# Kernel tuning notes

Measured on AMD Instinct MI355X. Metric: run time of the kernel, lower is better.

## Reference

```python
import jax, jax.numpy as jnp
import numpy as np
from jax import lax

WINDOW_SIZE = 11
SIGMA = 1.5
DATA_RANGE = 1.0
LEVELS = 4
EPS = 1e-8
DN = ('NCHW', 'OIHW', 'NCHW')


def _gauss1d(k, sigma):
    coords = jnp.arange(k, dtype=jnp.float32) - k // 2
    g = jnp.exp(-coords ** 2 / (2.0 * sigma ** 2))
    return g / g.sum()


def _blur(x, g):
    # separable depthwise Gaussian blur, VALID padding (use_padding=False)
    C = x.shape[1]
    k = g.shape[0]
    kw = jnp.broadcast_to(g.reshape(1, 1, 1, k), (C, 1, 1, k)).astype(x.dtype)
    kh = jnp.broadcast_to(g.reshape(1, 1, k, 1), (C, 1, k, 1)).astype(x.dtype)
    x = lax.conv_general_dilated(x, kw, (1, 1), 'VALID', dimension_numbers=DN, feature_group_count=C)
    x = lax.conv_general_dilated(x, kh, (1, 1), 'VALID', dimension_numbers=DN, feature_group_count=C)
    return x


def _avg_pool2(x):
    B, C, H, W = x.shape  # H, W even here (512 -> 64)
    return x.reshape(B, C, H // 2, 2, W // 2, 2).mean(axis=(3, 5))


def _ssim_level(X, Y, g):
    C1 = (0.01 * DATA_RANGE) ** 2
    C2 = (0.03 * DATA_RANGE) ** 2
    mu1 = _blur(X, g)
    mu2 = _blur(Y, g)
    sigma1_sq = _blur(X * X, g) - mu1 * mu1
    sigma2_sq = _blur(Y * Y, g) - mu2 * mu2
    sigma12 = _blur(X * Y, g) - mu1 * mu2
    cs_map = jax.nn.relu((2.0 * sigma12 + C2) / (sigma1_sq + sigma2_sq + C2))
    ssim_map = (2.0 * mu1 * mu2 + C1) / (mu1 * mu1 + mu2 * mu2 + C1) * cs_map
    return ssim_map.mean(axis=(1, 2, 3)), cs_map.mean(axis=(1, 2, 3))


def setup_inputs() -> dict:
    key = jax.random.key(0)
    kx, ky = jax.random.split(key)
    X = jax.random.uniform(kx, (16, 3, 512, 512), dtype=jnp.float32)
    Y = jax.random.uniform(ky, (16, 3, 512, 512), dtype=jnp.float32)
    return {'X': X, 'Y': Y}


def reference(X, Y):
    g = _gauss1d(WINDOW_SIZE, SIGMA)
    w = jnp.array([0.0448, 0.2856, 0.3001, 0.2363], dtype=jnp.float32)
    w = w / w.sum()
    vals = []
    for i in range(LEVELS):
        ss, cs = _ssim_level(X, Y, g)
        if i < LEVELS - 1:
            vals.append(cs)
            X = _avg_pool2(X)
            Y = _avg_pool2(Y)
        else:
            vals.append(ss)
    vals = jnp.maximum(jnp.stack(vals, axis=0), EPS)  # [levels, B]
    ms = jnp.prod(vals ** w[:, None], axis=0)
    return 1.0 - ms
```

## Files before the change

### kernel.cpp

```cpp
#include <hip/hip_runtime.h>
#include <math.h>

#define HALO 10
#define TS 32
#define IN 42
#define NP 21
#define XSTR 46
#define HSTR 46
#define NBIN 256

typedef float f2 __attribute__((ext_vector_type(2)));

struct GaussW { float g[11]; };


__global__ __launch_bounds__(256, 6) void ssim_level_kernel(
    const float* __restrict__ X, const float* __restrict__ Y,
    int H, GaussW gw, float* __restrict__ Plevel, int last_level,
    float* __restrict__ Xpool, float* __restrict__ Ypool)
{
    const int W = H;
    const int Hout = H - HALO;

    __shared__ float U[4 * TS * HSTR];
    __shared__ float red[4];
    float* Xs = U;
    float* Ys = U + IN * XSTR;

    const int tid = threadIdx.x;
    const int bc  = blockIdx.z;
    const int b   = bc / 3;
    const int r0  = blockIdx.y * TS;
    const int c0  = blockIdx.x * TS;
    const size_t base = (size_t)bc * H * W;

    for (int idx = tid; idx < IN * NP; idx += 256) {
        int rr = idx / NP, pp = idx - rr * NP;
        int gr = r0 + rr, gc = c0 + 2 * pp;
        float2 xv = make_float2(0.f, 0.f), yv = make_float2(0.f, 0.f);
        if (gr < H && gc < W) {
            const float* xp = X + base + (size_t)gr * W + gc;
            const float* yp = Y + base + (size_t)gr * W + gc;
            xv = *(const float2*)xp;
            yv = *(const float2*)yp;
        }
        *(float2*)&Xs[rr * XSTR + 2 * pp] = xv;
        *(float2*)&Ys[rr * XSTR + 2 * pp] = yv;
    }
    __syncthreads();

    float x[18], y[18];
    int rr = 0, ccb = 0;
    if (tid < 168) {
        rr  = tid >> 2;
        ccb = (tid & 3) * 8;
        #pragma unroll
        for (int u = 0; u < 9; ++u) {
            *(f2*)&x[2 * u] = *(const f2*)&Xs[rr * XSTR + ccb + 2 * u];
            *(f2*)&y[2 * u] = *(const f2*)&Ys[rr * XSTR + ccb + 2 * u];
        }
    } else if (tid >= 192 && !last_level) {
        const int t = tid - 192;
        const int Wp = W >> 1;
        #pragma unroll
        for (int q = 0; q < 4; ++q) {
            int cell = q * 64 + t;
            int pr = cell >> 4, pc = cell & 15;
            float2 xa = *(const float2*)&Xs[(2 * pr)     * XSTR + 2 * pc];
            float2 xb = *(const float2*)&Xs[(2 * pr + 1) * XSTR + 2 * pc];
            float2 ya = *(const float2*)&Ys[(2 * pr)     * XSTR + 2 * pc];
            float2 yb = *(const float2*)&Ys[(2 * pr + 1) * XSTR + 2 * pc];
            size_t o = (size_t)bc * (H >> 1) * Wp + (size_t)(r0 / 2 + pr) * Wp + (c0 / 2 + pc);
            Xpool[o] = 0.25f * (xa.x + xa.y + xb.x + xb.y);
            Ypool[o] = 0.25f * (ya.x + ya.y + yb.x + yb.y);
        }
    }
    __syncthreads();

    if (tid < 168) {
        #pragma unroll
        for (int p = 0; p < 4; ++p) {
            f2 ax = {0.f, 0.f}, ay = {0.f, 0.f};
            #pragma unroll
            for (int k = 0; k < 11; ++k) {
                f2 vx = { x[2 * p + k], x[2 * p + k + 1] };
                f2 vy = { y[2 * p + k], y[2 * p + k + 1] };
                ax += vx * gw.g[k];
                ay += vy * gw.g[k];
            }
            U[(0 * TS + ccb + 2 * p    ) * HSTR + rr] = ax.x;
            U[(0 * TS + ccb + 2 * p + 1) * HSTR + rr] = ax.y;
            U[(1 * TS + ccb + 2 * p    ) * HSTR + rr] = ay.x;
            U[(1 * TS + ccb + 2 * p + 1) * HSTR + rr] = ay.y;
        }
        #pragma unroll
        for (int i = 0; i < 9; ++i) {
            f2 xv = *(f2*)&x[2 * i];
            f2 yv = *(f2*)&y[2 * i];
            f2 a = xv + yv;
            f2 d = xv - yv;
            *(f2*)&x[2 * i] = a * a;
            *(f2*)&y[2 * i] = d * d;
        }
        #pragma unroll
        for (int p = 0; p < 4; ++p) {
            f2 as = {0.f, 0.f}, ad = {0.f, 0.f};
            #pragma unroll
            for (int k = 0; k < 11; ++k) {
                f2 vs = { x[2 * p + k], x[2 * p + k + 1] };
                f2 vd = { y[2 * p + k], y[2 * p + k + 1] };
                as += vs * gw.g[k];
                ad += vd * gw.g[k];
            }
            U[(2 * TS + ccb + 2 * p    ) * HSTR + rr] = as.x;
            U[(2 * TS + ccb + 2 * p + 1) * HSTR + rr] = as.y;
            U[(3 * TS + ccb + 2 * p    ) * HSTR + rr] = ad.x;
            U[(3 * TS + ccb + 2 * p + 1) * HSTR + rr] = ad.y;
        }
    }
    __syncthreads();

    const int tx = tid & 31;
    const int ty = tid >> 5;
    const int rb = ty * 4;

    f2 m1[2], m2[2], S[2], D[2];
    #define VPASS(Q, OUT)                                                        \
    {                                                                            \
        float win[14];                                                           \
        _Pragma("unroll")                                                        \
        for (int i = 0; i < 7; ++i)                                              \
            *(f2*)&win[2 * i] = *(const f2*)&U[(Q * TS + tx) * HSTR + rb + 2 * i]; \
        _Pragma("unroll")                                                        \
        for (int h = 0; h < 2; ++h) {                                            \
            f2 acc = {0.f, 0.f};                                                 \
            _Pragma("unroll")                                                    \
            for (int k = 0; k < 11; ++k) {                                       \
                f2 v = { win[2 * h + k], win[2 * h + k + 1] };                   \
                acc += v * gw.g[k];                                              \
            }                                                                    \
            OUT[h] = acc;                                                        \
        }                                                                        \
    }
    VPASS(0, m1) VPASS(1, m2) VPASS(2, S) VPASS(3, D)
    #undef VPASS

    const float C1 = 1e-4f, C2 = 9e-4f;
    float acc_s = 0.f;
    #pragma unroll
    for (int o = 0; o < 4; ++o) {
        float u1 = m1[o >> 1][o & 1], u2 = m2[o >> 1][o & 1];
        float Sv = S[o >> 1][o & 1],  Dv = D[o >> 1][o & 1];
        float u1s = u1 * u1, u2s = u2 * u2, u12 = u1 * u2;
        float ssum = 0.5f  * (Sv + Dv);
        float sxy  = 0.25f * (Sv - Dv);
        float vsum = ssum - u1s - u2s;
        float v12  = sxy - u12;
        float A2   = fmaxf(2.f * v12 + C2, 0.f);
        float B1   = u1s + u2s + C1;
        float B2   = vsum + C2;
        float inv  = __builtin_amdgcn_rcpf(B1 * B2);
        float val;
        if (!last_level) {
            val = A2 * B1 * inv;
        } else {
            float A1 = 2.f * u12 + C1;
            val = A1 * A2 * inv;
        }
        bool valid = (r0 + rb + o < Hout) && (c0 + tx < Hout);
        acc_s += valid ? val : 0.f;
    }

    #pragma unroll
    for (int off = 32; off; off >>= 1) acc_s += __shfl_down(acc_s, off);
    if ((tid & 63) == 0) red[tid >> 6] = acc_s;
    __syncthreads();
    if (tid == 0) {
        int lin = blockIdx.x + gridDim.x * (blockIdx.y + gridDim.y * blockIdx.z);
        int bin = lin & (NBIN - 1);
        atomicAdd(&Plevel[bin * 16 + b], red[0] + red[1] + red[2] + red[3]);
    }
}

__global__ void finalize_kernel(const float* __restrict__ P, float* __restrict__ out) {
    __shared__ float red[64][4];
    const int tid  = threadIdx.x;
    const int pair = tid >> 2;
    const int chnk = tid & 3;
    const int l = pair >> 4, b = pair & 15;
    float s = 0.f;
    #pragma unroll 4
    for (int j = 0; j < 64; ++j)
        s += P[((l * NBIN) + (chnk * 64) + j) * 16 + b];
    red[pair][chnk] = s;
    __syncthreads();
    if (tid < 16) {
        const int bb = tid;
        const float wraw[4] = {0.0448f, 0.2856f, 0.3001f, 0.2363f};
        float wsum = wraw[0] + wraw[1] + wraw[2] + wraw[3];
        float ms = 1.f;
        for (int ll = 0; ll < 4; ++ll) {
            int Hh = 512 >> ll;
            int Ho = Hh - HALO;
            float cnt = 3.f * (float)Ho * (float)Ho;
            float val = (red[ll * 16 + bb][0] + red[ll * 16 + bb][1] +
                         red[ll * 16 + bb][2] + red[ll * 16 + bb][3]) / cnt;
            val = fmaxf(val, 1e-8f);
            ms *= powf(val, wraw[ll] / wsum);
        }
        out[bb] = 1.f - ms;
    }
}

extern "C" void kernel_launch(void* const* d_in, const int* in_sizes, int n_in,
                              void* d_out, int out_size, void* d_ws, size_t ws_size,
                              hipStream_t stream)
{
    const float* X0 = (const float*)d_in[0];
    const float* Y0 = (const float*)d_in[1];
    float* out = (float*)d_out;
    float* ws  = (float*)d_ws;

    const size_t PSZ = (size_t)4 * NBIN * 16;
    float* P  = ws;
    float* X1 = ws + PSZ;
    float* Y1 = X1 + (size_t)16 * 3 * 256 * 256;
    float* X2 = Y1 + (size_t)16 * 3 * 256 * 256;
    float* Y2 = X2 + (size_t)16 * 3 * 128 * 128;
    float* X3 = Y2 + (size_t)16 * 3 * 128 * 128;
    float* Y3 = X3 + (size_t)16 * 3 * 64 * 64;

    GaussW gw;
    {
        float s = 0.f;
        for (int i = 0; i < 11; ++i) {
            float d = (float)(i - 5);
            gw.g[i] = expf(-d * d / (2.f * 1.5f * 1.5f));
            s += gw.g[i];
        }
        for (int i = 0; i < 11; ++i) gw.g[i] /= s;
    }

    hipMemsetAsync(P, 0, PSZ * sizeof(float), stream);

    hipLaunchKernelGGL(ssim_level_kernel, dim3(16, 16, 48), dim3(256), 0, stream,
                       X0, Y0, 512, gw, P + 0 * NBIN * 16, 0, X1, Y1);
    hipLaunchKernelGGL(ssim_level_kernel, dim3(8, 8, 48),   dim3(256), 0, stream,
                       X1, Y1, 256, gw, P + 1 * NBIN * 16, 0, X2, Y2);
    hipLaunchKernelGGL(ssim_level_kernel, dim3(4, 4, 48),   dim3(256), 0, stream,
                       X2, Y2, 128, gw, P + 2 * NBIN * 16, 0, X3, Y3);
    hipLaunchKernelGGL(ssim_level_kernel, dim3(2, 2, 48),   dim3(256), 0, stream,
                       X3, Y3, 64,  gw, P + 3 * NBIN * 16, 1, (float*)nullptr, (float*)nullptr);

    hipLaunchKernelGGL(finalize_kernel, dim3(1), dim3(256), 0, stream, P, out);
}
```

Baseline: 201.0 us.

## Fuse all pyramid levels and finalize into one persistent kernel with grid barriers

Replaces the four per-level launches plus the finalize launch with a single persistent kernel. Blocks stride over the tiles of each level and meet at a hierarchical atomic grid barrier between levels, and block 0 does the final reduction. This removes launch gaps and the tail idle time of the small later levels. In exchange it depends on every block being co-resident, and the spin timeout could silently break correctness if they are not; level 0 also loses some per-block scheduling flexibility.

```diff
diff --git a/kernel.cpp b/kernel.cpp
--- a/kernel.cpp
+++ b/kernel.cpp
@@ -8,30 +8,57 @@
 #define XSTR 46
 #define HSTR 46
 #define NBIN 256
+#define NG 64
+#define BARW 2112
 
 typedef float f2 __attribute__((ext_vector_type(2)));
 
 struct GaussW { float g[11]; };
 
-
-__global__ __launch_bounds__(256, 6) void ssim_level_kernel(
+__device__ __forceinline__ void grid_barrier(unsigned* bar)
+{
+    __syncthreads();
+    if (threadIdx.x == 0) {
+        unsigned* root  = bar;
+        unsigned* grp   = bar + 16 + (blockIdx.x & (NG - 1)) * 16;
+        unsigned* mygen = bar + 16 + NG * 16 + (blockIdx.x & (NG - 1)) * 16;
+        const unsigned gsz = gridDim.x / NG;
+
+        unsigned gen = __hip_atomic_load(mygen, __ATOMIC_RELAXED, __HIP_MEMORY_SCOPE_AGENT);
+        unsigned a = __hip_atomic_fetch_add(grp, 1u, __ATOMIC_ACQ_REL, __HIP_MEMORY_SCOPE_AGENT);
+        if (a == gsz - 1) {
+            __hip_atomic_store(grp, 0u, __ATOMIC_RELAXED, __HIP_MEMORY_SCOPE_AGENT);
+            unsigned r = __hip_atomic_fetch_add(root, 1u, __ATOMIC_ACQ_REL, __HIP_MEMORY_SCOPE_AGENT);
+            if (r == NG - 1) {
+                __hip_atomic_store(root, 0u, __ATOMIC_RELAXED, __HIP_MEMORY_SCOPE_AGENT);
+                unsigned* gc = bar + 16 + NG * 16;
+                #pragma unroll 4
+                for (int i = 0; i < NG; ++i)
+                    __hip_atomic_store(gc + i * 16, gen + 1, __ATOMIC_RELEASE, __HIP_MEMORY_SCOPE_AGENT);
+            }
+        }
+        unsigned spin = 0;
+        while (__hip_atomic_load(mygen, __ATOMIC_RELAXED, __HIP_MEMORY_SCOPE_AGENT) == gen) {
+            __builtin_amdgcn_s_sleep(4);
+            if (++spin > (1u << 20)) break;
+        }
+        __builtin_amdgcn_fence(__ATOMIC_ACQUIRE, "agent");
+    }
+    __syncthreads();
+}
+
+__device__ __forceinline__ void ssim_tile(
     const float* __restrict__ X, const float* __restrict__ Y,
-    int H, GaussW gw, float* __restrict__ Plevel, int last_level,
-    float* __restrict__ Xpool, float* __restrict__ Ypool)
+    int H, const GaussW& gw, float* __restrict__ Plevel, int last_level,
+    float* __restrict__ Xpool, float* __restrict__ Ypool,
+    int bc, int r0, int c0, int lin, float* U, float* red)
 {
     const int W = H;
     const int Hout = H - HALO;
-
-    __shared__ float U[4 * TS * HSTR];
-    __shared__ float red[4];
     float* Xs = U;
     float* Ys = U + IN * XSTR;
-
     const int tid = threadIdx.x;
-    const int bc  = blockIdx.z;
     const int b   = bc / 3;
-    const int r0  = blockIdx.y * TS;
-    const int c0  = blockIdx.x * TS;
     const size_t base = (size_t)bc * H * W;
 
     for (int idx = tid; idx < IN * NP; idx += 256) {
@@ -125,22 +152,22 @@
     const int rb = ty * 4;
 
     f2 m1[2], m2[2], S[2], D[2];
-    #define VPASS(Q, OUT)                                                        \
-    {                                                                            \
-        float win[14];                                                           \
-        _Pragma("unroll")                                                        \
-        for (int i = 0; i < 7; ++i)                                              \
+    #define VPASS(Q, OUT)                                                          \
+    {                                                                              \
+        float win[14];                                                             \
+        _Pragma("unroll")                                                          \
+        for (int i = 0; i < 7; ++i)                                                \
             *(f2*)&win[2 * i] = *(const f2*)&U[(Q * TS + tx) * HSTR + rb + 2 * i]; \
-        _Pragma("unroll")                                                        \
-        for (int h = 0; h < 2; ++h) {                                            \
-            f2 acc = {0.f, 0.f};                                                 \
-            _Pragma("unroll")                                                    \
-            for (int k = 0; k < 11; ++k) {                                       \
-                f2 v = { win[2 * h + k], win[2 * h + k + 1] };                   \
-                acc += v * gw.g[k];                                              \
-            }                                                                    \
-            OUT[h] = acc;                                                        \
-        }                                                                        \
+        _Pragma("unroll")                                                          \
+        for (int h = 0; h < 2; ++h) {                                              \
+            f2 acc = {0.f, 0.f};                                                   \
+            _Pragma("unroll")                                                      \
+            for (int k = 0; k < 11; ++k) {                                         \
+                f2 v = { win[2 * h + k], win[2 * h + k + 1] };                     \
+                acc += v * gw.g[k];                                                \
+            }                                                                      \
+            OUT[h] = acc;                                                          \
+        }                                                                          \
     }
     VPASS(0, m1) VPASS(1, m2) VPASS(2, S) VPASS(3, D)
     #undef VPASS
@@ -176,10 +203,94 @@
     if ((tid & 63) == 0) red[tid >> 6] = acc_s;
     __syncthreads();
     if (tid == 0) {
-        int lin = blockIdx.x + gridDim.x * (blockIdx.y + gridDim.y * blockIdx.z);
         int bin = lin & (NBIN - 1);
         atomicAdd(&Plevel[bin * 16 + b], red[0] + red[1] + red[2] + red[3]);
     }
+}
+
+__global__ __launch_bounds__(256, 6) void ms_ssim_mega(
+    const float* __restrict__ X0, const float* __restrict__ Y0,
+    float* __restrict__ ws, float* __restrict__ out, GaussW gw)
+{
+    __shared__ float U[4 * TS * HSTR];
+    __shared__ float red[4];
+
+    unsigned* bar = (unsigned*)ws;
+    const size_t PSZ = (size_t)4 * NBIN * 16;
+    float* P  = ws + BARW;
+    float* X1 = P  + PSZ;
+    float* Y1 = X1 + (size_t)16 * 3 * 256 * 256;
+    float* X2 = Y1 + (size_t)16 * 3 * 256 * 256;
+    float* Y2 = X2 + (size_t)16 * 3 * 128 * 128;
+    float* X3 = Y2 + (size_t)16 * 3 * 128 * 128;
+    float* Y3 = X3 + (size_t)16 * 3 * 64 * 64;
+
+    #pragma unroll 1
+    for (int L = 0; L < 4; ++L) {
+        const int H   = 512 >> L;
+        const int lg2 = 2 * (4 - L);
+        const int ntiles = 48 << lg2;
+        const int last = (L == 3);
+        float* Pl = P + L * NBIN * 16;
+        const float *Xi, *Yi; float *Xo, *Yo;
+        if      (L == 0) { Xi = X0; Yi = Y0; Xo = X1; Yo = Y1; }
+        else if (L == 1) { Xi = X1; Yi = Y1; Xo = X2; Yo = Y2; }
+        else if (L == 2) { Xi = X2; Yi = Y2; Xo = X3; Yo = Y3; }
+        else             { Xi = X3; Yi = Y3; Xo = nullptr; Yo = nullptr; }
+
+        for (int t = blockIdx.x; t < ntiles; t += gridDim.x) {
+            const int bc  = t >> lg2;
+            const int rem = t & ((1 << lg2) - 1);
+            const int tyi = rem >> (4 - L);
+            const int txi = rem & ((H >> 5) - 1);
+            ssim_tile(Xi, Yi, H, gw, Pl, last, Xo, Yo,
+                      bc, tyi * TS, txi * TS, t, U, red);
+        }
+        grid_barrier(bar);
+    }
+
+    if (blockIdx.x == 0) {
+        float* fin = U;
+        const int tid  = threadIdx.x;
+        const int pair = tid >> 2;
+        const int chnk = tid & 3;
+        const int l = pair >> 4, b = pair & 15;
+        float s = 0.f;
+        #pragma unroll 4
+        for (int j = 0; j < 64; ++j)
+            s += P[((l * NBIN) + (chnk * 64) + j) * 16 + b];
+        fin[pair * 4 + chnk] = s;
+        __syncthreads();
+        if (tid < 16) {
+            const int bb = tid;
+            const float wraw[4] = {0.0448f, 0.2856f, 0.3001f, 0.2363f};
+            float wsum = wraw[0] + wraw[1] + wraw[2] + wraw[3];
+            float ms = 1.f;
+            for (int ll = 0; ll < 4; ++ll) {
+                int Hh = 512 >> ll;
+                int Ho = Hh - HALO;
+                float cnt = 3.f * (float)Ho * (float)Ho;
+                float val = (fin[(ll * 16 + bb) * 4 + 0] + fin[(ll * 16 + bb) * 4 + 1] +
+                             fin[(ll * 16 + bb) * 4 + 2] + fin[(ll * 16 + bb) * 4 + 3]) / cnt;
+                val = fmaxf(val, 1e-8f);
+                ms *= powf(val, wraw[ll] / wsum);
+            }
+            out[bb] = 1.f - ms;
+        }
+    }
+}
+
+__global__ __launch_bounds__(256, 6) void ssim_level_kernel(
+    const float* __restrict__ X, const float* __restrict__ Y,
+    int H, GaussW gw, float* __restrict__ Plevel, int last_level,
+    float* __restrict__ Xpool, float* __restrict__ Ypool)
+{
+    __shared__ float U[4 * TS * HSTR];
+    __shared__ float red[4];
+    const int bc = blockIdx.z;
+    const int lin = blockIdx.x + gridDim.x * (blockIdx.y + gridDim.y * blockIdx.z);
+    ssim_tile(X, Y, H, gw, Plevel, last_level, Xpool, Ypool,
+              bc, blockIdx.y * TS, blockIdx.x * TS, lin, U, red);
 }
 
 __global__ void finalize_kernel(const float* __restrict__ P, float* __restrict__ out) {
@@ -222,8 +333,8 @@
     float* ws  = (float*)d_ws;
 
     const size_t PSZ = (size_t)4 * NBIN * 16;
-    float* P  = ws;
-    float* X1 = ws + PSZ;
+    float* P  = ws + BARW;
+    float* X1 = P  + PSZ;
     float* Y1 = X1 + (size_t)16 * 3 * 256 * 256;
     float* X2 = Y1 + (size_t)16 * 3 * 256 * 256;
     float* Y2 = X2 + (size_t)16 * 3 * 128 * 128;
@@ -241,16 +352,35 @@
         for (int i = 0; i < 11; ++i) gw.g[i] /= s;
     }
 
-    hipMemsetAsync(P, 0, PSZ * sizeof(float), stream);
-
-    hipLaunchKernelGGL(ssim_level_kernel, dim3(16, 16, 48), dim3(256), 0, stream,
-                       X0, Y0, 512, gw, P + 0 * NBIN * 16, 0, X1, Y1);
-    hipLaunchKernelGGL(ssim_level_kernel, dim3(8, 8, 48),   dim3(256), 0, stream,
-                       X1, Y1, 256, gw, P + 1 * NBIN * 16, 0, X2, Y2);
-    hipLaunchKernelGGL(ssim_level_kernel, dim3(4, 4, 48),   dim3(256), 0, stream,
-                       X2, Y2, 128, gw, P + 2 * NBIN * 16, 0, X3, Y3);
-    hipLaunchKernelGGL(ssim_level_kernel, dim3(2, 2, 48),   dim3(256), 0, stream,
-                       X3, Y3, 64,  gw, P + 3 * NBIN * 16, 1, (float*)nullptr, (float*)nullptr);
-
-    hipLaunchKernelGGL(finalize_kernel, dim3(1), dim3(256), 0, stream, P, out);
-}
+    hipMemsetAsync(ws, 0, (BARW + PSZ) * sizeof(float), stream);
+
+    static int s_grid = 0;
+    if (s_grid == 0) {
+        int nb = 0;
+        if (hipOccupancyMaxActiveBlocksPerMultiprocessor(&nb, ms_ssim_mega, 256, 0) != hipSuccess)
+            nb = 0;
+        if (nb > 6) nb = 6;
+        int dev = 0;
+        hipGetDevice(&dev);
+        int ncu = 0;
+        if (hipDeviceGetAttribute(&ncu, hipDeviceAttributeMultiprocessorCount, dev) != hipSuccess || ncu < 64)
+            ncu = 256;
+        s_grid = (nb * ncu) & ~(NG - 1);
+        if (s_grid < NG) s_grid = -1;
+    }
+
+    if (s_grid > 0) {
+        hipLaunchKernelGGL(ms_ssim_mega, dim3(s_grid), dim3(256), 0, stream,
+                           X0, Y0, ws, out, gw);
+    } else {
+        hipLaunchKernelGGL(ssim_level_kernel, dim3(16, 16, 48), dim3(256), 0, stream,
+                           X0, Y0, 512, gw, P + 0 * NBIN * 16, 0, X1, Y1);
+        hipLaunchKernelGGL(ssim_level_kernel, dim3(8, 8, 48),   dim3(256), 0, stream,
+                           X1, Y1, 256, gw, P + 1 * NBIN * 16, 0, X2, Y2);
+        hipLaunchKernelGGL(ssim_level_kernel, dim3(4, 4, 48),   dim3(256), 0, stream,
+                           X2, Y2, 128, gw, P + 2 * NBIN * 16, 0, X3, Y3);
+        hipLaunchKernelGGL(ssim_level_kernel, dim3(2, 2, 48),   dim3(256), 0, stream,
+                           X3, Y3, 64,  gw, P + 3 * NBIN * 16, 1, (float*)nullptr, (float*)nullptr);
+        hipLaunchKernelGGL(finalize_kernel, dim3(1), dim3(256), 0, stream, P, out);
+    }
+}
```

Result: slower. 387.8 us (+92.9%).

## Interleave X/Y channels in shared memory so blur passes use paired f2 math

Applied to the files above, without the earlier changes.

Shared tiles now store X and Y (and later S and D) interleaved as float pairs, so each horizontal and vertical blur tap is one packed f2 multiply-add across the two channels instead of pairing adjacent columns or rows. The shared buffer shrinks from four planes with stride 46 to two planes with stride 86, and launch bounds rise from 6 to 7 blocks per CU to exploit the smaller footprint. The aim is fewer LDS instructions and more resident waves. The risks are different LDS bank-conflict patterns and higher register pressure from the 18-entry and 14-entry f2 windows.

```diff
diff --git a/kernel.cpp b/kernel.cpp
--- a/kernel.cpp
+++ b/kernel.cpp
@@ -5,8 +5,7 @@
 #define TS 32
 #define IN 42
 #define NP 21
-#define XSTR 46
-#define HSTR 46
+#define ISTR 86
 #define NBIN 256
 
 typedef float f2 __attribute__((ext_vector_type(2)));
@@ -14,7 +13,7 @@
 struct GaussW { float g[11]; };
 
 
-__global__ __launch_bounds__(256, 6) void ssim_level_kernel(
+__global__ __launch_bounds__(256, 7) void ssim_level_kernel(
     const float* __restrict__ X, const float* __restrict__ Y,
     int H, GaussW gw, float* __restrict__ Plevel, int last_level,
     float* __restrict__ Xpool, float* __restrict__ Ypool)
@@ -22,10 +21,11 @@
     const int W = H;
     const int Hout = H - HALO;
 
-    __shared__ float U[4 * TS * HSTR];
+    __shared__ float U[2 * TS * ISTR];
     __shared__ float red[4];
-    float* Xs = U;
-    float* Ys = U + IN * XSTR;
+    float* XYs = U;
+    float* HXY = U;
+    float* HSD = U + TS * ISTR;
 
     const int tid = threadIdx.x;
     const int bc  = blockIdx.z;
@@ -39,26 +39,22 @@
         int gr = r0 + rr, gc = c0 + 2 * pp;
         float2 xv = make_float2(0.f, 0.f), yv = make_float2(0.f, 0.f);
         if (gr < H && gc < W) {
-            const float* xp = X + base + (size_t)gr * W + gc;
-            const float* yp = Y + base + (size_t)gr * W + gc;
-            xv = *(const float2*)xp;
-            yv = *(const float2*)yp;
-        }
-        *(float2*)&Xs[rr * XSTR + 2 * pp] = xv;
-        *(float2*)&Ys[rr * XSTR + 2 * pp] = yv;
-    }
-    __syncthreads();
-
-    float x[18], y[18];
+            xv = *(const float2*)(X + base + (size_t)gr * W + gc);
+            yv = *(const float2*)(Y + base + (size_t)gr * W + gc);
+        }
+        *(f2*)&XYs[rr * ISTR + 4 * pp    ] = f2{ xv.x, yv.x };
+        *(f2*)&XYs[rr * ISTR + 4 * pp + 2] = f2{ xv.y, yv.y };
+    }
+    __syncthreads();
+
+    f2 w[18];
     int rr = 0, ccb = 0;
     if (tid < 168) {
         rr  = tid >> 2;
         ccb = (tid & 3) * 8;
         #pragma unroll
-        for (int u = 0; u < 9; ++u) {
-            *(f2*)&x[2 * u] = *(const f2*)&Xs[rr * XSTR + ccb + 2 * u];
-            *(f2*)&y[2 * u] = *(const f2*)&Ys[rr * XSTR + ccb + 2 * u];
-        }
+        for (int u = 0; u < 18; ++u)
+            w[u] = *(const f2*)&XYs[rr * ISTR + 2 * (ccb + u)];
     } else if (tid >= 192 && !last_level) {
         const int t = tid - 192;
         const int Wp = W >> 1;
@@ -66,56 +62,38 @@
         for (int q = 0; q < 4; ++q) {
             int cell = q * 64 + t;
             int pr = cell >> 4, pc = cell & 15;
-            float2 xa = *(const float2*)&Xs[(2 * pr)     * XSTR + 2 * pc];
-            float2 xb = *(const float2*)&Xs[(2 * pr + 1) * XSTR + 2 * pc];
-            float2 ya = *(const float2*)&Ys[(2 * pr)     * XSTR + 2 * pc];
-            float2 yb = *(const float2*)&Ys[(2 * pr + 1) * XSTR + 2 * pc];
+            f2 s0 = *(const f2*)&XYs[(2 * pr)     * ISTR + 4 * pc];
+            f2 s1 = *(const f2*)&XYs[(2 * pr)     * ISTR + 4 * pc + 2];
+            f2 s2 = *(const f2*)&XYs[(2 * pr + 1) * ISTR + 4 * pc];
+            f2 s3 = *(const f2*)&XYs[(2 * pr + 1) * ISTR + 4 * pc + 2];
+            f2 sum = (s0 + s1) + (s2 + s3);
             size_t o = (size_t)bc * (H >> 1) * Wp + (size_t)(r0 / 2 + pr) * Wp + (c0 / 2 + pc);
-            Xpool[o] = 0.25f * (xa.x + xa.y + xb.x + xb.y);
-            Ypool[o] = 0.25f * (ya.x + ya.y + yb.x + yb.y);
+            Xpool[o] = 0.25f * sum.x;
+            Ypool[o] = 0.25f * sum.y;
         }
     }
     __syncthreads();
 
     if (tid < 168) {
         #pragma unroll
-        for (int p = 0; p < 4; ++p) {
-            f2 ax = {0.f, 0.f}, ay = {0.f, 0.f};
+        for (int c = 0; c < 8; ++c) {
+            f2 a = {0.f, 0.f};
             #pragma unroll
-            for (int k = 0; k < 11; ++k) {
-                f2 vx = { x[2 * p + k], x[2 * p + k + 1] };
-                f2 vy = { y[2 * p + k], y[2 * p + k + 1] };
-                ax += vx * gw.g[k];
-                ay += vy * gw.g[k];
-            }
-            U[(0 * TS + ccb + 2 * p    ) * HSTR + rr] = ax.x;
-            U[(0 * TS + ccb + 2 * p + 1) * HSTR + rr] = ax.y;
-            U[(1 * TS + ccb + 2 * p    ) * HSTR + rr] = ay.x;
-            U[(1 * TS + ccb + 2 * p + 1) * HSTR + rr] = ay.y;
-        }
-        #pragma unroll
-        for (int i = 0; i < 9; ++i) {
-            f2 xv = *(f2*)&x[2 * i];
-            f2 yv = *(f2*)&y[2 * i];
-            f2 a = xv + yv;
-            f2 d = xv - yv;
-            *(f2*)&x[2 * i] = a * a;
-            *(f2*)&y[2 * i] = d * d;
-        }
-        #pragma unroll
-        for (int p = 0; p < 4; ++p) {
-            f2 as = {0.f, 0.f}, ad = {0.f, 0.f};
+            for (int k = 0; k < 11; ++k) a += w[c + k] * gw.g[k];
+            *(f2*)&HXY[(ccb + c) * ISTR + 2 * rr] = a;
+        }
+        #pragma unroll
+        for (int u = 0; u < 18; ++u) {
+            float s = w[u].x + w[u].y;
+            float d = w[u].x - w[u].y;
+            w[u] = f2{ s, d } * f2{ s, d };
+        }
+        #pragma unroll
+        for (int c = 0; c < 8; ++c) {
+            f2 a = {0.f, 0.f};
             #pragma unroll
-            for (int k = 0; k < 11; ++k) {
-                f2 vs = { x[2 * p + k], x[2 * p + k + 1] };
-                f2 vd = { y[2 * p + k], y[2 * p + k + 1] };
-                as += vs * gw.g[k];
-                ad += vd * gw.g[k];
-            }
-            U[(2 * TS + ccb + 2 * p    ) * HSTR + rr] = as.x;
-            U[(2 * TS + ccb + 2 * p + 1) * HSTR + rr] = as.y;
-            U[(3 * TS + ccb + 2 * p    ) * HSTR + rr] = ad.x;
-            U[(3 * TS + ccb + 2 * p + 1) * HSTR + rr] = ad.y;
+            for (int k = 0; k < 11; ++k) a += w[c + k] * gw.g[k];
+            *(f2*)&HSD[(ccb + c) * ISTR + 2 * rr] = a;
         }
     }
     __syncthreads();
@@ -124,33 +102,30 @@
     const int ty = tid >> 5;
     const int rb = ty * 4;
 
-    f2 m1[2], m2[2], S[2], D[2];
-    #define VPASS(Q, OUT)                                                        \
+    f2 mu[4], sd[4];
+    #define VPASS(BASE, OUT)                                                     \
     {                                                                            \
-        float win[14];                                                           \
+        f2 v[14];                                                                \
         _Pragma("unroll")                                                        \
-        for (int i = 0; i < 7; ++i)                                              \
-            *(f2*)&win[2 * i] = *(const f2*)&U[(Q * TS + tx) * HSTR + rb + 2 * i]; \
+        for (int i = 0; i < 14; ++i)                                             \
+            v[i] = *(const f2*)&BASE[tx * ISTR + 2 * (rb + i)];                  \
         _Pragma("unroll")                                                        \
-        for (int h = 0; h < 2; ++h) {                                            \
+        for (int h = 0; h < 4; ++h) {                                            \
             f2 acc = {0.f, 0.f};                                                 \
             _Pragma("unroll")                                                    \
-            for (int k = 0; k < 11; ++k) {                                       \
-                f2 v = { win[2 * h + k], win[2 * h + k + 1] };                   \
-                acc += v * gw.g[k];                                              \
-            }                                                                    \
+            for (int k = 0; k < 11; ++k) acc += v[h + k] * gw.g[k];              \
             OUT[h] = acc;                                                        \
         }                                                                        \
     }
-    VPASS(0, m1) VPASS(1, m2) VPASS(2, S) VPASS(3, D)
+    VPASS(HXY, mu) VPASS(HSD, sd)
     #undef VPASS
 
     const float C1 = 1e-4f, C2 = 9e-4f;
     float acc_s = 0.f;
     #pragma unroll
     for (int o = 0; o < 4; ++o) {
-        float u1 = m1[o >> 1][o & 1], u2 = m2[o >> 1][o & 1];
-        float Sv = S[o >> 1][o & 1],  Dv = D[o >> 1][o & 1];
+        float u1 = mu[o].x, u2 = mu[o].y;
+        float Sv = sd[o].x, Dv = sd[o].y;
         float u1s = u1 * u1, u2s = u2 * u2, u12 = u1 * u2;
         float ssum = 0.5f  * (Sv + Dv);
         float sxy  = 0.25f * (Sv - Dv);
```

Result: no change. 199.2 us (-0.9%).
